# Performance work log

Measured on AMD Instinct MI355X. Metric: run time of the kernel, lower is better.

Reference implementation:

```python
import jax, jax.numpy as jnp
import numpy as np

B, C, L, H = 4, 512, 2048, 8
D = C // H  # head_dim


def setup_inputs() -> dict:
    key = jax.random.key(0)
    ks = jax.random.split(key, 9)
    s = 1.0 / np.sqrt(C)  # keep logits well-scaled like torch Linear init
    return {
        "x": jax.random.normal(ks[0], (B, C, L), dtype=jnp.float32),
        "Wq": jax.random.normal(ks[1], (C, C), dtype=jnp.float32) * s,
        "bq": jnp.zeros((C,), dtype=jnp.float32),
        "Wk": jax.random.normal(ks[2], (C, C), dtype=jnp.float32) * s,
        "bk": jnp.zeros((C,), dtype=jnp.float32),
        "Wv": jax.random.normal(ks[3], (C, C), dtype=jnp.float32) * s,
        "bv": jnp.zeros((C,), dtype=jnp.float32),
        "Wo": jax.random.normal(ks[4], (C, C), dtype=jnp.float32) * s,
        "bo": jnp.zeros((C,), dtype=jnp.float32),
    }


def reference(x, Wq, bq, Wk, bk, Wv, bv, Wo, bo):
    # x: (B, C, L) -> (B, L, C)
    xp = jnp.transpose(x, (0, 2, 1))
    scale = D ** (-0.5)

    def heads(w, b):
        y = xp @ w.T + b                      # (B, L, C)  torch Linear: x W^T + b
        return y.reshape(B, L, H, D).transpose(0, 2, 1, 3)  # (B, H, L, D)

    q = heads(Wq, bq)
    k = heads(Wk, bk)
    v = heads(Wv, bv)

    attn = jnp.einsum('bhqd,bhkd->bhqk', q, k) * scale  # (B, H, L, L)
    attn = jax.nn.softmax(attn, axis=-1)
    out = jnp.einsum('bhqk,bhkd->bhqd', attn, v)        # (B, H, L, D)
    out = out.transpose(0, 2, 1, 3).reshape(B, L, C)    # (B, L, C)
    out = out @ Wo.T + bo
    return x + jnp.transpose(out, (0, 2, 1))            # residual in (B, C, L)
```

## Files before the change

kernel.cpp:

```cpp
#include <hip/hip_runtime.h>
#include <math.h>

#define B_ 4
#define C_ 512
#define L_ 2048
#define H_ 8
#define D_ 64
#define QSCALE 0.18033688011112042f
#define DEFER_THR 12.0f

typedef __bf16 bf16x8 __attribute__((ext_vector_type(8)));
typedef float f32x4 __attribute__((ext_vector_type(4)));

__device__ __forceinline__ unsigned cvt_pk(float lo, float hi) {
    unsigned r;
    asm("v_cvt_pk_bf16_f32 %0, %1, %2" : "=v"(r) : "v"(lo), "v"(hi));
    return r;
}
__device__ __forceinline__ unsigned short f2bf_hw(float a) {
    unsigned r;
    asm("v_cvt_pk_bf16_f32 %0, %1, %1" : "=v"(r) : "v"(a));
    return (unsigned short)r;
}
__device__ __forceinline__ bf16x8 frag_ld(const unsigned short* p) {
    uint4 v = *reinterpret_cast<const uint4*>(p);
    return __builtin_bit_cast(bf16x8, v);
}
__device__ __forceinline__ float fmax3(float a, float b, float c) {
    return fmaxf(fmaxf(a, b), c);
}
__device__ __forceinline__ void glds16(const void* g, void* l) {
    __builtin_amdgcn_global_load_lds(
        (const __attribute__((address_space(1))) void*)g,
        (__attribute__((address_space(3))) void*)l, 16, 0, 0);
}

__global__ __launch_bounds__(256) void prep(
    const float* __restrict__ x,
    const float* __restrict__ w0, const float* __restrict__ w1,
    const float* __restrict__ w2, const float* __restrict__ w3,
    unsigned short* __restrict__ xt,
    unsigned short* __restrict__ o0, unsigned short* __restrict__ o1,
    unsigned short* __restrict__ o2, unsigned short* __restrict__ o3)
{
    __shared__ float T[64][68];
    const int t = threadIdx.x;

    if (blockIdx.z < B_) {
        const int b  = blockIdx.z;
        const int l0 = blockIdx.x * 64;
        const int c0 = blockIdx.y * 64;
        const float* xb = x + (size_t)b * C_ * L_;
        unsigned short* xtb = xt + (size_t)b * L_ * C_;

        #pragma unroll
        for (int p = 0; p < 4; ++p) {
            const int ci = 16 * p + (t >> 4);
            const int l4 = (t & 15) * 4;
            *reinterpret_cast<float4*>(&T[ci][l4]) =
                *reinterpret_cast<const float4*>(xb + (size_t)(c0 + ci) * L_ + l0 + l4);
        }
        __syncthreads();

        const int lo = t >> 2;
        const int cb = (t & 3) * 16;
        unsigned w[8];
        #pragma unroll
        for (int k = 0; k < 8; ++k)
            w[k] = cvt_pk(T[cb + 2 * k][lo], T[cb + 2 * k + 1][lo]);
        unsigned short* dst = xtb + (size_t)(l0 + lo) * C_ + c0 + cb;
        *reinterpret_cast<uint4*>(dst)     = make_uint4(w[0], w[1], w[2], w[3]);
        *reinterpret_cast<uint4*>(dst + 8) = make_uint4(w[4], w[5], w[6], w[7]);
    } else {
        const int m = blockIdx.z - B_;
        const float* src; unsigned short* dst;
        if      (m == 0) { src = w0; dst = o0; }
        else if (m == 1) { src = w1; dst = o1; }
        else if (m == 2) { src = w2; dst = o2; }
        else             { src = w3; dst = o3; }
        const int flat = blockIdx.x + 32 * blockIdx.y;
        const size_t idx = ((size_t)flat * 256 + t) * 4;
        const float4 v = *reinterpret_cast<const float4*>(src + idx);
        *reinterpret_cast<uint2*>(dst + idx) =
            make_uint2(cvt_pk(v.x, v.y), cvt_pk(v.z, v.w));
    }
}

__global__ __launch_bounds__(256) void qkv_gemm(
    const unsigned short* __restrict__ xt,
    const unsigned short* __restrict__ wq, const unsigned short* __restrict__ wk,
    const unsigned short* __restrict__ wv,
    const float* __restrict__ bq, const float* __restrict__ bk,
    const float* __restrict__ bv,
    unsigned short* __restrict__ qb, unsigned short* __restrict__ kb,
    unsigned short* __restrict__ vb)
{
    __shared__ unsigned short As[128][32];
    __shared__ unsigned short Bs[128][32];

    const int mode = blockIdx.z >> 2;
    const int b    = blockIdx.z & 3;
    const size_t LC = (size_t)L_ * C_;

    const unsigned short *A, *Bt;
    const float* bias;
    unsigned short* Out;
    float scale = 1.0f;
    int m0, n0, oN, biasN;
    if (mode == 0) {
        A = xt + (size_t)b * LC; Bt = wq; bias = bq; Out = qb + (size_t)b * LC;
        m0 = blockIdx.y * 128; n0 = blockIdx.x * 128; oN = C_; biasN = 1;
        scale = QSCALE;
    } else if (mode == 1) {
        A = xt + (size_t)b * LC; Bt = wk; bias = bk; Out = kb + (size_t)b * LC;
        m0 = blockIdx.y * 128; n0 = blockIdx.x * 128; oN = C_; biasN = 1;
    } else {
        A = wv; Bt = xt + (size_t)b * LC; bias = bv; Out = vb + (size_t)b * LC;
        m0 = blockIdx.x * 128; n0 = blockIdx.y * 128; oN = L_; biasN = 0;
    }

    const int t = threadIdx.x;
    const int lane = t & 63, wid = t >> 6;
    const int wm = (wid >> 1) * 64, wn = (wid & 1) * 64;
    const int q16 = lane & 15, g = lane >> 4;

    const int gr = wid * 32 + (lane >> 2);
    const int gc = (lane & 3) * 8;
    const unsigned short* Ap0 = A  + (size_t)(m0 + gr) * C_ + gc;
    const unsigned short* Ap1 = Ap0 + 16 * C_;
    const unsigned short* Bp0 = Bt + (size_t)(n0 + gr) * C_ + gc;
    const unsigned short* Bp1 = Bp0 + 16 * C_;
    unsigned short* lA0 = &As[wid * 32][0];
    unsigned short* lA1 = &As[wid * 32 + 16][0];
    unsigned short* lB0 = &Bs[wid * 32][0];
    unsigned short* lB1 = &Bs[wid * 32 + 16][0];

    f32x4 zero4 = {0.f, 0.f, 0.f, 0.f};
    f32x4 acc[4][4];
    #pragma unroll
    for (int i = 0; i < 4; ++i)
        #pragma unroll
        for (int j = 0; j < 4; ++j) acc[i][j] = zero4;

    for (int k0 = 0; k0 < C_; k0 += 32) {
        __syncthreads();
        glds16(Ap0 + k0, lA0); glds16(Ap1 + k0, lA1);
        glds16(Bp0 + k0, lB0); glds16(Bp1 + k0, lB1);
        __syncthreads();
        bf16x8 af[4], bfr[4];
        #pragma unroll
        for (int i = 0; i < 4; ++i) af[i]  = frag_ld(&As[wm + 16 * i + q16][8 * g]);
        #pragma unroll
        for (int j = 0; j < 4; ++j) bfr[j] = frag_ld(&Bs[wn + 16 * j + q16][8 * g]);
        #pragma unroll
        for (int i = 0; i < 4; ++i)
            #pragma unroll
            for (int j = 0; j < 4; ++j)
                acc[i][j] = __builtin_amdgcn_mfma_f32_16x16x32_bf16(
                    af[i], bfr[j], acc[i][j], 0, 0, 0);
    }

    #pragma unroll
    for (int j = 0; j < 4; ++j) {
        const int n = n0 + wn + 16 * j + q16;
        const float bn = biasN ? bias[n] : 0.f;
        #pragma unroll
        for (int i = 0; i < 4; ++i) {
            #pragma unroll
            for (int r = 0; r < 4; ++r) {
                const int m = m0 + wm + 16 * i + 4 * g + r;
                const float v = acc[i][j][r] + (biasN ? bn : bias[m]);
                Out[(size_t)m * oN + n] = f2bf_hw(v * scale);
            }
        }
    }
}

__global__ __launch_bounds__(256) void gemm_out(
    const unsigned short* __restrict__ A,
    const unsigned short* __restrict__ Bt,
    const float* __restrict__ bias,
    float* __restrict__ Out, const float* __restrict__ resid)
{
    __shared__ unsigned short As[128][40];
    __shared__ unsigned short Bs[128][40];

    const int bz = blockIdx.z;
    const size_t LC = (size_t)L_ * C_;
    Bt    += (size_t)bz * LC;
    Out   += (size_t)bz * LC;
    resid += (size_t)bz * LC;

    const int n0 = blockIdx.x * 128;
    const int m0 = blockIdx.y * 128;
    const int t  = threadIdx.x;
    const int lane = t & 63, wid = t >> 6;
    const int wm = (wid >> 1) * 64, wn = (wid & 1) * 64;
    const int q16 = lane & 15, g = lane >> 4;

    const int srow = t >> 1;
    const int scol = (t & 1) * 16;
    const unsigned short* Ap = A  + (size_t)(m0 + srow) * C_ + scol;
    const unsigned short* Bp = Bt + (size_t)(n0 + srow) * C_ + scol;

    f32x4 zero4 = {0.f, 0.f, 0.f, 0.f};
    f32x4 acc[4][4];
    #pragma unroll
    for (int i = 0; i < 4; ++i)
        #pragma unroll
        for (int j = 0; j < 4; ++j) acc[i][j] = zero4;

    uint4 ar0 = *reinterpret_cast<const uint4*>(Ap);
    uint4 ar1 = *reinterpret_cast<const uint4*>(Ap + 8);
    uint4 br0 = *reinterpret_cast<const uint4*>(Bp);
    uint4 br1 = *reinterpret_cast<const uint4*>(Bp + 8);

    for (int k0 = 0; k0 < C_; k0 += 32) {
        __syncthreads();
        *reinterpret_cast<uint4*>(&As[srow][scol])     = ar0;
        *reinterpret_cast<uint4*>(&As[srow][scol + 8]) = ar1;
        *reinterpret_cast<uint4*>(&Bs[srow][scol])     = br0;
        *reinterpret_cast<uint4*>(&Bs[srow][scol + 8]) = br1;
        __syncthreads();
        if (k0 + 32 < C_) {
            ar0 = *reinterpret_cast<const uint4*>(Ap + k0 + 32);
            ar1 = *reinterpret_cast<const uint4*>(Ap + k0 + 40);
            br0 = *reinterpret_cast<const uint4*>(Bp + k0 + 32);
            br1 = *reinterpret_cast<const uint4*>(Bp + k0 + 40);
        }
        bf16x8 af[4], bfr[4];
        #pragma unroll
        for (int i = 0; i < 4; ++i) af[i]  = frag_ld(&As[wm + 16 * i + q16][8 * g]);
        #pragma unroll
        for (int j = 0; j < 4; ++j) bfr[j] = frag_ld(&Bs[wn + 16 * j + q16][8 * g]);
        #pragma unroll
        for (int i = 0; i < 4; ++i)
            #pragma unroll
            for (int j = 0; j < 4; ++j)
                acc[i][j] = __builtin_amdgcn_mfma_f32_16x16x32_bf16(
                    af[i], bfr[j], acc[i][j], 0, 0, 0);
    }

    #pragma unroll
    for (int j = 0; j < 4; ++j) {
        const int n = n0 + wn + 16 * j + q16;
        #pragma unroll
        for (int i = 0; i < 4; ++i) {
            #pragma unroll
            for (int r = 0; r < 4; ++r) {
                const int m = m0 + wm + 16 * i + 4 * g + r;
                const size_t off = (size_t)m * L_ + n;
                Out[off] = acc[i][j][r] + bias[m] + resid[off];
            }
        }
    }
}

__global__ __launch_bounds__(256) void attn_mfma(
    const unsigned short* __restrict__ Qb,
    const unsigned short* __restrict__ Kb,
    const unsigned short* __restrict__ Vb,
    unsigned short* __restrict__ Ab)
{
    __shared__ unsigned short Ks[64][72];
    __shared__ unsigned short Vs[64][72];
    __shared__ unsigned short Pw[4][16][64];

    const int q0 = blockIdx.x * 64;
    const int h  = blockIdx.y;
    const int b  = blockIdx.z;
    const int t  = threadIdx.x, lane = t & 63, wid = t >> 6;
    const int q16 = lane & 15, g = lane >> 4;
    const int h4 = (q16 & 7) << 2;

    const unsigned short* Qg = Qb + (size_t)b * L_ * C_;
    const unsigned short* Kg = Kb + (size_t)b * L_ * C_;
    const unsigned short* Vg = Vb + ((size_t)b * C_ + h * D_) * L_;
    unsigned short* Ag       = Ab + (size_t)b * L_ * C_;

    unsigned* pw = reinterpret_cast<unsigned*>(&Pw[wid][q16][0]);

    bf16x8 qf[2];
    {
        const unsigned short* qp =
            Qg + (size_t)(q0 + 16 * wid + q16) * C_ + h * D_ + 8 * g;
        qf[0] = frag_ld(qp);
        qf[1] = frag_ld(qp + 32);
    }

    f32x4 zero4 = {0.f, 0.f, 0.f, 0.f};
    f32x4 oacc[4];
    #pragma unroll
    for (int n = 0; n < 4; ++n) oacc[n] = zero4;
    float m_s = -INFINITY;
    float l_p = 0.f;

    const int sr = t >> 2;
    const int sc = (t & 3) * 16;

    uint4 kr0, kr1, vr0, vr1;
    {
        const unsigned short* kp = Kg + (size_t)sr * C_ + h * D_ + sc;
        kr0 = *reinterpret_cast<const uint4*>(kp);
        kr1 = *reinterpret_cast<const uint4*>(kp + 8);
        const unsigned short* vp = Vg + (size_t)sr * L_ + sc;
        vr0 = *reinterpret_cast<const uint4*>(vp);
        vr1 = *reinterpret_cast<const uint4*>(vp + 8);
    }

    for (int kt = 0; kt < 32; ++kt) {
        __syncthreads();
        *reinterpret_cast<uint4*>(&Ks[sr][sc])     = kr0;
        *reinterpret_cast<uint4*>(&Ks[sr][sc + 8]) = kr1;
        *reinterpret_cast<uint4*>(&Vs[sr][sc])     = vr0;
        *reinterpret_cast<uint4*>(&Vs[sr][sc + 8]) = vr1;
        __syncthreads();
        if (kt + 1 < 32) {
            const int kn = (kt + 1) * 64;
            const unsigned short* kp = Kg + (size_t)(kn + sr) * C_ + h * D_ + sc;
            kr0 = *reinterpret_cast<const uint4*>(kp);
            kr1 = *reinterpret_cast<const uint4*>(kp + 8);
            const unsigned short* vp = Vg + (size_t)sr * L_ + kn + sc;
            vr0 = *reinterpret_cast<const uint4*>(vp);
            vr1 = *reinterpret_cast<const uint4*>(vp + 8);
        }

        f32x4 sacc[4];
        #pragma unroll
        for (int f = 0; f < 4; ++f) sacc[f] = zero4;
        #pragma unroll
        for (int s = 0; s < 2; ++s) {
            #pragma unroll
            for (int f = 0; f < 4; ++f) {
                bf16x8 kf = frag_ld(&Ks[16 * f + q16][32 * s + 8 * g]);
                sacc[f] = __builtin_amdgcn_mfma_f32_16x16x32_bf16(
                    kf, qf[s], sacc[f], 0, 0, 0);
            }
        }

        const float t0 = fmax3(sacc[0][0], sacc[0][1], sacc[0][2]);
        const float t1 = fmax3(sacc[0][3], sacc[1][0], sacc[1][1]);
        const float t2 = fmax3(sacc[1][2], sacc[1][3], sacc[2][0]);
        const float t3 = fmax3(sacc[2][1], sacc[2][2], sacc[2][3]);
        const float t4 = fmax3(sacc[3][0], sacc[3][1], sacc[3][2]);
        float pm = fmaxf(fmax3(t0, t1, t2), fmax3(t3, t4, sacc[3][3]));
        pm = fmaxf(pm, __shfl_xor(pm, 16));
        pm = fmaxf(pm, __shfl_xor(pm, 32));

        if (!__all(pm - m_s <= DEFER_THR)) {
            const float mn   = fmaxf(m_s, pm);
            const float corr = exp2f(m_s - mn);
            m_s = mn;
            l_p *= corr;
            #pragma unroll
            for (int r = 0; r < 4; ++r) {
                const float c_o = __shfl(corr, 20 * g + r);
                #pragma unroll
                for (int n = 0; n < 4; ++n) oacc[n][r] *= c_o;
            }
        }

        float p[4][4];
        #pragma unroll
        for (int f = 0; f < 4; ++f) {
            #pragma unroll
            for (int r = 0; r < 4; ++r) p[f][r] = exp2f(sacc[f][r] - m_s);
            l_p += (p[f][0] + p[f][1]) + (p[f][2] + p[f][3]);
        }

        #pragma unroll
        for (int f = 0; f < 4; ++f) {
            uint2 v2;
            v2.x = cvt_pk(p[f][0], p[f][1]);
            v2.y = cvt_pk(p[f][2], p[f][3]);
            *reinterpret_cast<uint2*>(pw + ((8 * f + 2 * g) ^ h4)) = v2;
        }

        #pragma unroll
        for (int s2 = 0; s2 < 2; ++s2) {
            bf16x8 pf = frag_ld(reinterpret_cast<const unsigned short*>(
                pw + ((16 * s2 + 4 * g) ^ h4)));
            #pragma unroll
            for (int n = 0; n < 4; ++n) {
                bf16x8 vf = frag_ld(&Vs[16 * n + q16][32 * s2 + 8 * g]);
                oacc[n] = __builtin_amdgcn_mfma_f32_16x16x32_bf16(
                    pf, vf, oacc[n], 0, 0, 0);
            }
        }
    }

    float lr = l_p;
    lr += __shfl_xor(lr, 16);
    lr += __shfl_xor(lr, 32);
    #pragma unroll
    for (int r = 0; r < 4; ++r) {
        const float l_o = __shfl(lr, 20 * g + r);
        const float inv = 1.f / l_o;
        const int q = q0 + 16 * wid + 4 * g + r;
        #pragma unroll
        for (int n = 0; n < 4; ++n)
            Ag[(size_t)q * C_ + h * D_ + 16 * n + q16] = f2bf_hw(oacc[n][r] * inv);
    }
}

extern "C" void kernel_launch(void* const* d_in, const int* in_sizes, int n_in,
                              void* d_out, int out_size, void* d_ws, size_t ws_size,
                              hipStream_t stream)
{
    const float* x  = (const float*)d_in[0];
    const float* Wq = (const float*)d_in[1];
    const float* bq = (const float*)d_in[2];
    const float* Wk = (const float*)d_in[3];
    const float* bk = (const float*)d_in[4];
    const float* Wv = (const float*)d_in[5];
    const float* bv = (const float*)d_in[6];
    const float* Wo = (const float*)d_in[7];
    const float* bo = (const float*)d_in[8];
    float* out = (float*)d_out;

    const size_t NB = (size_t)B_ * L_ * C_;
    const size_t NW = (size_t)C_ * C_;
    unsigned short* ws16 = (unsigned short*)d_ws;
    unsigned short* xt  = ws16;
    unsigned short* qb  = xt  + NB;
    unsigned short* kb  = qb  + NB;
    unsigned short* vb  = kb  + NB;
    unsigned short* att = vb  + NB;
    unsigned short* wqb = att + NB;
    unsigned short* wkb = wqb + NW;
    unsigned short* wvb = wkb + NW;
    unsigned short* wob = wvb + NW;

    prep<<<dim3(32, 8, 2 * B_), 256, 0, stream>>>(
        x, Wq, Wk, Wv, Wo, xt, wqb, wkb, wvb, wob);

    qkv_gemm<<<dim3(4, 16, 3 * B_), 256, 0, stream>>>(
        xt, wqb, wkb, wvb, bq, bk, bv, qb, kb, vb);

    attn_mfma<<<dim3(L_ / 64, H_, B_), 256, 0, stream>>>(qb, kb, vb, att);

    gemm_out<<<dim3(16, 4, B_), 256, 0, stream>>>(wob, att, bo, out, x);
}
```

Measured before the change: 211.1 us.

## Double-buffer LDS with async global-to-LDS loads, swizzle K/V, and compute row sums via MFMA

```diff
diff --git a/kernel.cpp b/kernel.cpp
--- a/kernel.cpp
+++ b/kernel.cpp
@@ -95,8 +95,8 @@
     unsigned short* __restrict__ qb, unsigned short* __restrict__ kb,
     unsigned short* __restrict__ vb)
 {
-    __shared__ unsigned short As[128][32];
-    __shared__ unsigned short Bs[128][32];
+    __shared__ unsigned short As[2][128][32];
+    __shared__ unsigned short Bs[2][128][32];
 
     const int mode = blockIdx.z >> 2;
     const int b    = blockIdx.z & 3;
@@ -118,6 +118,7 @@
         A = wv; Bt = xt + (size_t)b * LC; bias = bv; Out = vb + (size_t)b * LC;
         m0 = blockIdx.x * 128; n0 = blockIdx.y * 128; oN = L_; biasN = 0;
     }
+    const int doswz = (mode != 0);
 
     const int t = threadIdx.x;
     const int lane = t & 63, wid = t >> 6;
@@ -130,10 +131,6 @@
     const unsigned short* Ap1 = Ap0 + 16 * C_;
     const unsigned short* Bp0 = Bt + (size_t)(n0 + gr) * C_ + gc;
     const unsigned short* Bp1 = Bp0 + 16 * C_;
-    unsigned short* lA0 = &As[wid * 32][0];
-    unsigned short* lA1 = &As[wid * 32 + 16][0];
-    unsigned short* lB0 = &Bs[wid * 32][0];
-    unsigned short* lB1 = &Bs[wid * 32 + 16][0];
 
     f32x4 zero4 = {0.f, 0.f, 0.f, 0.f};
     f32x4 acc[4][4];
@@ -142,22 +139,32 @@
         #pragma unroll
         for (int j = 0; j < 4; ++j) acc[i][j] = zero4;
 
-    for (int k0 = 0; k0 < C_; k0 += 32) {
-        __syncthreads();
-        glds16(Ap0 + k0, lA0); glds16(Ap1 + k0, lA1);
-        glds16(Bp0 + k0, lB0); glds16(Bp1 + k0, lB1);
-        __syncthreads();
+    glds16(Ap0, &As[0][wid * 32][0]);      glds16(Ap1, &As[0][wid * 32 + 16][0]);
+    glds16(Bp0, &Bs[0][wid * 32][0]);      glds16(Bp1, &Bs[0][wid * 32 + 16][0]);
+    __syncthreads();
+
+    #pragma unroll 2
+    for (int it = 0; it < 16; ++it) {
+        const int cur = it & 1;
+        if (it < 15) {
+            const int ko = (it + 1) * 32;
+            glds16(Ap0 + ko, &As[cur ^ 1][wid * 32][0]);
+            glds16(Ap1 + ko, &As[cur ^ 1][wid * 32 + 16][0]);
+            glds16(Bp0 + ko, &Bs[cur ^ 1][wid * 32][0]);
+            glds16(Bp1 + ko, &Bs[cur ^ 1][wid * 32 + 16][0]);
+        }
         bf16x8 af[4], bfr[4];
         #pragma unroll
-        for (int i = 0; i < 4; ++i) af[i]  = frag_ld(&As[wm + 16 * i + q16][8 * g]);
-        #pragma unroll
-        for (int j = 0; j < 4; ++j) bfr[j] = frag_ld(&Bs[wn + 16 * j + q16][8 * g]);
+        for (int i = 0; i < 4; ++i) af[i]  = frag_ld(&As[cur][wm + 16 * i + q16][8 * g]);
+        #pragma unroll
+        for (int j = 0; j < 4; ++j) bfr[j] = frag_ld(&Bs[cur][wn + 16 * j + q16][8 * g]);
         #pragma unroll
         for (int i = 0; i < 4; ++i)
             #pragma unroll
             for (int j = 0; j < 4; ++j)
                 acc[i][j] = __builtin_amdgcn_mfma_f32_16x16x32_bf16(
                     af[i], bfr[j], acc[i][j], 0, 0, 0);
+        __syncthreads();
     }
 
     #pragma unroll
@@ -170,7 +177,8 @@
             for (int r = 0; r < 4; ++r) {
                 const int m = m0 + wm + 16 * i + 4 * g + r;
                 const float v = acc[i][j][r] + (biasN ? bn : bias[m]);
-                Out[(size_t)m * oN + n] = f2bf_hw(v * scale);
+                const int nn = doswz ? (n ^ ((m & 7) << 3)) : n;
+                Out[(size_t)m * oN + nn] = f2bf_hw(v * scale);
             }
         }
     }
@@ -262,8 +270,8 @@
     const unsigned short* __restrict__ Vb,
     unsigned short* __restrict__ Ab)
 {
-    __shared__ unsigned short Ks[64][72];
-    __shared__ unsigned short Vs[64][72];
+    __shared__ unsigned short Ks[2][64][64];
+    __shared__ unsigned short Vs[2][64][64];
     __shared__ unsigned short Pw[4][16][64];
 
     const int q0 = blockIdx.x * 64;
@@ -271,10 +279,11 @@
     const int b  = blockIdx.z;
     const int t  = threadIdx.x, lane = t & 63, wid = t >> 6;
     const int q16 = lane & 15, g = lane >> 4;
-    const int h4 = (q16 & 7) << 2;
+    const int swz = (q16 & 7) << 3;
+    const int h4  = (q16 & 7) << 2;
 
     const unsigned short* Qg = Qb + (size_t)b * L_ * C_;
-    const unsigned short* Kg = Kb + (size_t)b * L_ * C_;
+    const unsigned short* Kg = Kb + (size_t)b * L_ * C_ + h * D_;
     const unsigned short* Vg = Vb + ((size_t)b * C_ + h * D_) * L_;
     unsigned short* Ag       = Ab + (size_t)b * L_ * C_;
 
@@ -288,41 +297,38 @@
         qf[1] = frag_ld(qp + 32);
     }
 
+    const unsigned ow = (q16 == 0) ? 0x3F803F80u : 0u;
+    const uint4 ov = make_uint4(ow, ow, ow, ow);
+    const bf16x8 onesf = __builtin_bit_cast(bf16x8, ov);
+
     f32x4 zero4 = {0.f, 0.f, 0.f, 0.f};
-    f32x4 oacc[4];
+    f32x4 oacc[4], lacc = zero4;
     #pragma unroll
     for (int n = 0; n < 4; ++n) oacc[n] = zero4;
     float m_s = -INFINITY;
-    float l_p = 0.f;
-
-    const int sr = t >> 2;
-    const int sc = (t & 3) * 16;
-
-    uint4 kr0, kr1, vr0, vr1;
-    {
-        const unsigned short* kp = Kg + (size_t)sr * C_ + h * D_ + sc;
-        kr0 = *reinterpret_cast<const uint4*>(kp);
-        kr1 = *reinterpret_cast<const uint4*>(kp + 8);
-        const unsigned short* vp = Vg + (size_t)sr * L_ + sc;
-        vr0 = *reinterpret_cast<const uint4*>(vp);
-        vr1 = *reinterpret_cast<const uint4*>(vp + 8);
-    }
-
+
+    const int gr8 = lane >> 3;
+    const int gc8 = (lane & 7) * 8;
+    const unsigned short* Kp0 = Kg + (size_t)(16 * wid     + gr8) * C_ + gc8;
+    const unsigned short* Kp1 = Kg + (size_t)(16 * wid + 8 + gr8) * C_ + gc8;
+    const unsigned short* Vp0 = Vg + (size_t)(16 * wid     + gr8) * L_ + gc8;
+    const unsigned short* Vp1 = Vg + (size_t)(16 * wid + 8 + gr8) * L_ + gc8;
+
+    glds16(Kp0, &Ks[0][16 * wid][0]);
+    glds16(Kp1, &Ks[0][16 * wid + 8][0]);
+    glds16(Vp0, &Vs[0][16 * wid][0]);
+    glds16(Vp1, &Vs[0][16 * wid + 8][0]);
+    __syncthreads();
+
+    #pragma unroll 2
     for (int kt = 0; kt < 32; ++kt) {
-        __syncthreads();
-        *reinterpret_cast<uint4*>(&Ks[sr][sc])     = kr0;
-        *reinterpret_cast<uint4*>(&Ks[sr][sc + 8]) = kr1;
-        *reinterpret_cast<uint4*>(&Vs[sr][sc])     = vr0;
-        *reinterpret_cast<uint4*>(&Vs[sr][sc + 8]) = vr1;
-        __syncthreads();
-        if (kt + 1 < 32) {
-            const int kn = (kt + 1) * 64;
-            const unsigned short* kp = Kg + (size_t)(kn + sr) * C_ + h * D_ + sc;
-            kr0 = *reinterpret_cast<const uint4*>(kp);
-            kr1 = *reinterpret_cast<const uint4*>(kp + 8);
-            const unsigned short* vp = Vg + (size_t)sr * L_ + kn + sc;
-            vr0 = *reinterpret_cast<const uint4*>(vp);
-            vr1 = *reinterpret_cast<const uint4*>(vp + 8);
+        const int cur = kt & 1;
+        if (kt < 31) {
+            const size_t ko = (size_t)(kt + 1) * 64;
+            glds16(Kp0 + ko * C_, &Ks[cur ^ 1][16 * wid][0]);
+            glds16(Kp1 + ko * C_, &Ks[cur ^ 1][16 * wid + 8][0]);
+            glds16(Vp0 + ko,      &Vs[cur ^ 1][16 * wid][0]);
+            glds16(Vp1 + ko,      &Vs[cur ^ 1][16 * wid + 8][0]);
         }
 
         f32x4 sacc[4];
@@ -332,7 +338,7 @@
         for (int s = 0; s < 2; ++s) {
             #pragma unroll
             for (int f = 0; f < 4; ++f) {
-                bf16x8 kf = frag_ld(&Ks[16 * f + q16][32 * s + 8 * g]);
+                bf16x8 kf = frag_ld(&Ks[cur][16 * f + q16][(32 * s + 8 * g) ^ swz]);
                 sacc[f] = __builtin_amdgcn_mfma_f32_16x16x32_bf16(
                     kf, qf[s], sacc[f], 0, 0, 0);
             }
@@ -351,22 +357,20 @@
             const float mn   = fmaxf(m_s, pm);
             const float corr = exp2f(m_s - mn);
             m_s = mn;
-            l_p *= corr;
             #pragma unroll
             for (int r = 0; r < 4; ++r) {
                 const float c_o = __shfl(corr, 20 * g + r);
                 #pragma unroll
                 for (int n = 0; n < 4; ++n) oacc[n][r] *= c_o;
+                lacc[r] *= c_o;
             }
         }
 
         float p[4][4];
         #pragma unroll
-        for (int f = 0; f < 4; ++f) {
+        for (int f = 0; f < 4; ++f)
             #pragma unroll
             for (int r = 0; r < 4; ++r) p[f][r] = exp2f(sacc[f][r] - m_s);
-            l_p += (p[f][0] + p[f][1]) + (p[f][2] + p[f][3]);
-        }
 
         #pragma unroll
         for (int f = 0; f < 4; ++f) {
@@ -382,19 +386,20 @@
                 pw + ((16 * s2 + 4 * g) ^ h4)));
             #pragma unroll
             for (int n = 0; n < 4; ++n) {
-                bf16x8 vf = frag_ld(&Vs[16 * n + q16][32 * s2 + 8 * g]);
+                bf16x8 vf = frag_ld(&Vs[cur][16 * n + q16][(32 * s2 + 8 * g) ^ swz]);
                 oacc[n] = __builtin_amdgcn_mfma_f32_16x16x32_bf16(
                     pf, vf, oacc[n], 0, 0, 0);
             }
-        }
-    }
-
-    float lr = l_p;
-    lr += __shfl_xor(lr, 16);
-    lr += __shfl_xor(lr, 32);
+            lacc = __builtin_amdgcn_mfma_f32_16x16x32_bf16(
+                pf, onesf, lacc, 0, 0, 0);
+        }
+
+        __syncthreads();
+    }
+
     #pragma unroll
     for (int r = 0; r < 4; ++r) {
-        const float l_o = __shfl(lr, 20 * g + r);
+        const float l_o = __shfl(lacc[r], lane & 48);
         const float inv = 1.f / l_o;
         const int q = q0 + 16 * wid + 4 * g + r;
         #pragma unroll
```

Measured after the change: 225.1 us. 1.07x slower.
